# Kernel optimization log

Hardware: AMD Instinct MI355X
Metric: run time of the kernel (lower is better)

## Reference

```python
import jax, jax.numpy as jnp
import numpy as np

L, V, D, S_MAX, B, S, H = 8, 32000, 1024, 1024, 4, 1024, 16
FF = 4 * D
EPS = 1e-5


def setup_inputs() -> dict:
    key = jax.random.key(0)
    ks = jax.random.split(key, 20)
    g = lambda k, shape: jax.random.normal(k, shape, dtype=jnp.float32) * 0.02
    inp = {
        'tokens': jax.random.randint(ks[0], (B, S), 0, V, dtype=jnp.int32),
        'num_heads': H,
        'emb': g(ks[1], (V, D)),
        'pos_emb': g(ks[2], (S_MAX, D)),
        'Wq': g(ks[3], (L, D, D)), 'bq': jnp.zeros((L, D), jnp.float32),
        'Wk': g(ks[4], (L, D, D)), 'bk': jnp.zeros((L, D), jnp.float32),
        'Wv': g(ks[5], (L, D, D)), 'bv': jnp.zeros((L, D), jnp.float32),
        'Wo': g(ks[6], (L, D, D)), 'bo': jnp.zeros((L, D), jnp.float32),
        'n1_s': jnp.ones((L, D), jnp.float32), 'n1_b': jnp.zeros((L, D), jnp.float32),
        'W1': g(ks[7], (L, D, FF)), 'b1': jnp.zeros((L, FF), jnp.float32),
        'W2': g(ks[8], (L, FF, D)), 'b2': jnp.zeros((L, D), jnp.float32),
        'n2_s': jnp.ones((L, D), jnp.float32), 'n2_b': jnp.zeros((L, D), jnp.float32),
    }
    return inp


def _layernorm(x, s, b):
    mu = jnp.mean(x, axis=-1, keepdims=True)
    var = jnp.mean(jnp.square(x - mu), axis=-1, keepdims=True)
    return s * (x - mu) * jax.lax.rsqrt(var + EPS) + b


def _forward(tokens, num_heads, emb, pos_emb, Wq, bq, Wk, bk, Wv, bv, Wo, bo,
             n1_s, n1_b, W1, b1, W2, b2, n2_s, n2_b):
    Bn, Sn = tokens.shape
    d = emb.shape[1]
    hd = d // num_heads
    x = emb[tokens] + pos_emb[:Sn][None, :, :]  # [B,S,D]

    def split_heads(t):  # [B,S,D] -> [B,H,S,hd]
        return t.reshape(Bn, Sn, num_heads, hd).transpose(0, 2, 1, 3)

    causal = jnp.triu(jnp.ones((Sn, Sn), dtype=bool), k=1)
    scale = 1.0 / np.sqrt(hd)
    nlayers = Wq.shape[0]
    for l in range(nlayers):
        q = split_heads(x @ Wq[l] + bq[l])
        k = split_heads(x @ Wk[l] + bk[l])
        v = split_heads(x @ Wv[l] + bv[l])
        scores = jnp.einsum('bhqd,bhkd->bhqk', q, k) * scale
        scores = jnp.where(causal, -jnp.inf, scores)
        attn = jax.nn.softmax(scores, axis=-1)
        ctx = jnp.einsum('bhqk,bhkd->bhqd', attn, v)
        ctx = ctx.transpose(0, 2, 1, 3).reshape(Bn, Sn, d)
        x = _layernorm(x + (ctx @ Wo[l] + bo[l]), n1_s[l], n1_b[l])
        h = jax.nn.relu(x @ W1[l] + b1[l])
        x = _layernorm(x + (h @ W2[l] + b2[l]), n2_s[l], n2_b[l])
    return x @ emb.T  # tied output head -> [B,S,V]


def reference(tokens, num_heads, emb, pos_emb, Wq, bq, Wk, bk, Wv, bv, Wo, bo,
              n1_s, n1_b, W1, b1, W2, b2, n2_s, n2_b):
    return _forward(tokens, num_heads, emb, pos_emb, Wq, bq, Wk, bk, Wv, bv,
                    Wo, bo, n1_s, n1_b, W1, b1, W2, b2, n2_s, n2_b)
```

## Files before the change

### kernel.cpp

```cpp
#include <hip/hip_runtime.h>

#define D_MODEL 1024
#define SEQ     1024
#define BATCH   4
#define NHEAD   16
#define HDIM    64
#define FF_DIM  4096
#define NLAYER  8
#define VOCAB   32000
#define ROWS    (BATCH*SEQ)
#define QKV_N   3072
#define LN_EPS  1e-5f

typedef __attribute__((ext_vector_type(4))) float   f32x4;
typedef __attribute__((ext_vector_type(8))) unsigned short u16x8;
typedef __attribute__((ext_vector_type(8))) __bf16  bf16x8;

typedef const unsigned int __attribute__((address_space(1)))* gas_t;
typedef unsigned int __attribute__((address_space(3)))* las_t;

__device__ __forceinline__ void gld16(const void* g, void* l) {
    __builtin_amdgcn_global_load_lds((gas_t)g, (las_t)l, 16, 0, 0);
}

__device__ __forceinline__ unsigned short f2bf(float f) {
    unsigned int u = __builtin_bit_cast(unsigned int, f);
    u += 0x7FFFu + ((u >> 16) & 1u);
    return (unsigned short)(u >> 16);
}

__device__ __forceinline__ float bf2f(unsigned short u) {
    return __builtin_bit_cast(float, (unsigned int)u << 16);
}

__device__ __forceinline__ f32x4 mfma32(u16x8 a, u16x8 b, f32x4 c) {
    return __builtin_amdgcn_mfma_f32_16x16x32_bf16(
        __builtin_bit_cast(bf16x8, a), __builtin_bit_cast(bf16x8, b), c, 0, 0, 0);
}

__global__ __launch_bounds__(256) void embed_k(
    const int* __restrict__ tok, const float* __restrict__ emb,
    const float* __restrict__ pos, unsigned short* __restrict__ xb)
{
    int bs = blockIdx.x;
    int s  = bs & (SEQ - 1);
    int tk = tok[bs];
    int c  = threadIdx.x * 4;
    float4 e = *(const float4*)(emb + (size_t)tk * D_MODEL + c);
    float4 p = *(const float4*)(pos + (size_t)s * D_MODEL + c);
    float y0 = e.x + p.x, y1 = e.y + p.y, y2 = e.z + p.z, y3 = e.w + p.w;
    size_t base = (size_t)bs * D_MODEL + c;
    unsigned long long pk = (unsigned long long)f2bf(y0)
        | ((unsigned long long)f2bf(y1) << 16)
        | ((unsigned long long)f2bf(y2) << 32)
        | ((unsigned long long)f2bf(y3) << 48);
    *(unsigned long long*)(xb + base) = pk;
}

__global__ __launch_bounds__(256) void cast_bf(
    const float* __restrict__ in, unsigned short* __restrict__ out, size_t n)
{
    size_t i = ((size_t)blockIdx.x * 256 + threadIdx.x) * 4;
    if (i >= n) return;
    float4 v = *(const float4*)(in + i);
    unsigned long long pk = (unsigned long long)f2bf(v.x)
        | ((unsigned long long)f2bf(v.y) << 16)
        | ((unsigned long long)f2bf(v.z) << 32)
        | ((unsigned long long)f2bf(v.w) << 48);
    *(unsigned long long*)(out + i) = pk;
}

__global__ __launch_bounds__(256) void bias3_k(
    const float* __restrict__ bq, const float* __restrict__ bk,
    const float* __restrict__ bv, float* __restrict__ out)
{
    int l = blockIdx.x / 3, which = blockIdx.x % 3;
    const float* src = which == 0 ? bq : (which == 1 ? bk : bv);
    int i = threadIdx.x * 4;
    float4 v = *(const float4*)(src + (size_t)l * D_MODEL + i);
    *(float4*)(out + (size_t)l * QKV_N + which * D_MODEL + i) = v;
}

__device__ __forceinline__ void tc_tile(
    const float* __restrict__ W, unsigned short* __restrict__ Wt,
    int K, int N, int n0, int k0)
{
    __shared__ float t[64][65];
    int rr = threadIdx.x >> 4;
    int cc = (threadIdx.x & 15) * 4;
#pragma unroll
    for (int it = 0; it < 4; it++) {
        int r = it * 16 + rr;
        float4 v = *(const float4*)(W + (size_t)(k0 + r) * N + n0 + cc);
        t[r][cc] = v.x; t[r][cc + 1] = v.y; t[r][cc + 2] = v.z; t[r][cc + 3] = v.w;
    }
    __syncthreads();
#pragma unroll
    for (int it = 0; it < 4; it++) {
        int n = it * 16 + rr;
        unsigned long long pk = (unsigned long long)f2bf(t[cc][n])
            | ((unsigned long long)f2bf(t[cc + 1][n]) << 16)
            | ((unsigned long long)f2bf(t[cc + 2][n]) << 32)
            | ((unsigned long long)f2bf(t[cc + 3][n]) << 48);
        *(unsigned long long*)(Wt + (size_t)(n0 + n) * K + k0 + cc) = pk;
    }
}

__global__ __launch_bounds__(256) void transpose_all(
    const float* __restrict__ Wq, const float* __restrict__ Wk,
    const float* __restrict__ Wv, const float* __restrict__ Wo,
    const float* __restrict__ W1, const float* __restrict__ W2,
    unsigned short* __restrict__ wt)
{
    int b = blockIdx.x;
    const float* W; unsigned short* out; int K, N, t;
    if (b < 768)       { int w = b >> 8; t = b & 255; W = w == 0 ? Wq : (w == 1 ? Wk : Wv);
                         out = wt + (size_t)w * 1048576; K = 1024; N = 1024; }
    else if (b < 1024) { t = b - 768;  W = Wo; out = wt + (size_t)3 * 1048576; K = 1024; N = 1024; }
    else if (b < 2048) { t = b - 1024; W = W1; out = wt + (size_t)4 * 1048576; K = 1024; N = 4096; }
    else               { t = b - 2048; W = W2; out = wt + (size_t)8 * 1048576; K = 4096; N = 1024; }
    int ntx = N >> 6;
    tc_tile(W, out, K, N, (t % ntx) * 64, (t / ntx) * 64);
}

template<int MODE>
__global__ __launch_bounds__(256, 3) void gemm_bt(
    const unsigned short* __restrict__ A, int lda,
    const unsigned short* __restrict__ Bt, int ldb,
    const float* __restrict__ bias, void* __restrict__ Cout, int N, int Klen)
{
    __shared__ unsigned short As[128 * 32];
    __shared__ unsigned short Bs[128 * 32];
    const int part = blockIdx.y;
    A  += (size_t)part * Klen;
    Bt += (size_t)part * Klen;
    int flat = blockIdx.x;
    const int bm = flat & 31, bn = flat >> 5;
    const int tid  = threadIdx.x;
    const int wid  = tid >> 6, lane = tid & 63;
    const int l16  = lane & 15, lhi = lane >> 4;
    const int wr   = wid >> 1, wc = wid & 1;

    const int srow = wid * 32 + (lane >> 2);
    const int scol = (lane & 3) * 8;
    const unsigned short* gA0 = A  + ((size_t)bm * 128 + srow) * lda + scol;
    const unsigned short* gB0 = Bt + ((size_t)bn * 128 + srow) * ldb + scol;
    unsigned short* lA = As + wid * 32 * 32;
    unsigned short* lB = Bs + wid * 32 * 32;

    f32x4 acc[4][4];
#pragma unroll
    for (int i = 0; i < 4; i++)
#pragma unroll
        for (int j = 0; j < 4; j++) acc[i][j] = (f32x4){0.f, 0.f, 0.f, 0.f};

    for (int k0 = 0; k0 < Klen; k0 += 32) {
        __syncthreads();
        gld16(gA0 + k0,                    lA);
        gld16(gA0 + k0 + 16 * (size_t)lda, lA + 16 * 32);
        gld16(gB0 + k0,                    lB);
        gld16(gB0 + k0 + 16 * (size_t)ldb, lB + 16 * 32);
        __syncthreads();
        u16x8 af[4], bfr[4];
#pragma unroll
        for (int i = 0; i < 4; i++)
            af[i] = *(const u16x8*)(As + (wr * 64 + i * 16 + l16) * 32 + lhi * 8);
#pragma unroll
        for (int i = 0; i < 4; i++)
            bfr[i] = *(const u16x8*)(Bs + (wc * 64 + i * 16 + l16) * 32 + lhi * 8);
#pragma unroll
        for (int mi = 0; mi < 4; mi++)
#pragma unroll
            for (int ni = 0; ni < 4; ni++)
                acc[mi][ni] = mfma32(af[mi], bfr[ni], acc[mi][ni]);
    }

    const size_t pofs = (size_t)part * (size_t)ROWS * N;
#pragma unroll
    for (int mi = 0; mi < 4; mi++) {
        float bv[4];
#pragma unroll
        for (int ni = 0; ni < 4; ni++)
            bv[ni] = (bias && part == 0) ? bias[bn * 128 + wc * 64 + ni * 16 + l16] : 0.f;
#pragma unroll
        for (int j = 0; j < 4; j++) {
            int row = bm * 128 + wr * 64 + mi * 16 + lhi * 4 + j;
#pragma unroll
            for (int ni = 0; ni < 4; ni++) {
                int col = bn * 128 + wc * 64 + ni * 16 + l16;
                float v = acc[mi][ni][j] + bv[ni];
                size_t idx = pofs + (size_t)row * N + col;
                if constexpr (MODE == 1) {
                    ((unsigned short*)Cout)[idx] = f2bf(v);
                } else {
                    ((unsigned short*)Cout)[idx] = f2bf(v > 0.f ? v : 0.f);
                }
            }
        }
    }
}

#define PSYNC() do { __builtin_amdgcn_s_barrier(); \
    asm volatile("s_waitcnt lgkmcnt(0)" ::: "memory"); \
    __builtin_amdgcn_sched_barrier(0); } while (0)
#define PEND() __builtin_amdgcn_s_barrier()
#define VM4()  asm volatile("s_waitcnt vmcnt(4)" ::: "memory")

#define LOADA(reg, half) do { \
    _Pragma("unroll") \
    for (int m_ = 0; m_ < 4; m_++) { \
        aF[m_][0] = *(const u16x8*)((reg) + ((half)*4 + m_) * 2048 + lane0); \
        aF[m_][1] = *(const u16x8*)((reg) + ((half)*4 + m_) * 2048 + lane1); \
    } } while (0)

#define LOADB(reg, np) do { \
    _Pragma("unroll") \
    for (int n_ = 0; n_ < 2; n_++) { \
        bF[(np)*2 + n_][0] = *(const u16x8*)((reg) + ((np)*2 + n_) * 2048 + lane0); \
        bF[(np)*2 + n_][1] = *(const u16x8*)((reg) + ((np)*2 + n_) * 2048 + lane1); \
    } } while (0)

#define MFMA8(ma, np) do { \
    __builtin_amdgcn_s_setprio(1); \
    _Pragma("unroll") \
    for (int m_ = 0; m_ < 4; m_++) \
        _Pragma("unroll") \
        for (int n_ = 0; n_ < 2; n_++) { \
            acc[(ma)+m_][(np)*2+n_] = mfma32(aF[m_][0], bF[(np)*2+n_][0], acc[(ma)+m_][(np)*2+n_]); \
            acc[(ma)+m_][(np)*2+n_] = mfma32(aF[m_][1], bF[(np)*2+n_][1], acc[(ma)+m_][(np)*2+n_]); \
        } \
    __builtin_amdgcn_s_setprio(0); \
} while (0)

template<int MODE, int SWZ>
__global__ __launch_bounds__(512, 2) void gemm256(
    const unsigned short* __restrict__ A, int lda,
    const unsigned short* __restrict__ Bt, int ldb,
    const float* __restrict__ bias, void* __restrict__ Cout, int N, int Klen)
{
    __shared__ unsigned short lds[65536] __attribute__((aligned(128)));
    const int tid = threadIdx.x, wid = tid >> 6, lane = tid & 63;
    const int l16 = lane & 15, lhi = lane >> 4;
    const int wr = wid >> 2, wc = wid & 3;

    const int part = blockIdx.y;
    A  += (size_t)part * Klen;
    Bt += (size_t)part * Klen;

    int flat = blockIdx.x;
    if constexpr (SWZ) {
        int cpx = gridDim.x >> 3; flat = (flat & 7) * cpx + (flat >> 3);
    }
    const int bm = flat & 15, bn = flat >> 4;
    const int NT = Klen >> 6;

    const int srowL = tid >> 3;
    const int scolb = ((tid & 7) << 4) ^ (((tid >> 3) & 7) << 4);
    const unsigned short* baseA = A  + (size_t)(bm * 256 + srowL) * lda + (scolb >> 1);
    const unsigned short* baseB = Bt + (size_t)(bn * 256 + srowL) * ldb + (scolb >> 1);
    unsigned short* dst0 = lds + wid * 512;

    auto stage = [&](int isB, int tile, int h) {
        const size_t ld = isB ? (size_t)ldb : (size_t)lda;
        const unsigned short* s = (isB ? baseB : baseA) + (size_t)(h * 128) * ld + (size_t)tile * 64;
        unsigned short* d = dst0 + (tile & 1) * 32768 + isB * 16384 + h * 8192;
        gld16(s, d);
        gld16(s + 64 * ld, d + 4096);
    };

    const int lswz  = (l16 & 7) << 4;
    const int lane0 = ((lhi * 16) ^ lswz) + l16 * 128;
    const int lane1 = ((64 + lhi * 16) ^ lswz) + l16 * 128;

    const char* aR0 = (const char*)lds + wr * 16384;
    const char* bR0 = (const char*)lds + 32768 + (wc >> 1) * 16384 + (wc & 1) * 8192;
    const char* aR1 = aR0 + 65536;
    const char* bR1 = bR0 + 65536;

    f32x4 acc[8][4];
#pragma unroll
    for (int i = 0; i < 8; i++)
#pragma unroll
        for (int j = 0; j < 4; j++) acc[i][j] = (f32x4){0.f, 0.f, 0.f, 0.f};
    u16x8 aF[4][2], bF[4][2];

    stage(1, 0, 0); stage(1, 0, 1);
    stage(0, 0, 0); stage(0, 0, 1);
    stage(1, 1, 0); stage(1, 1, 1);
    VM4();
    __builtin_amdgcn_s_barrier();

    for (int t = 0; t < NT; t += 2) {
        const bool more = (t + 2) < NT;
        LOADA(aR0, 0); LOADB(bR0, 0); stage(0, t + 1, 0);
        PSYNC(); MFMA8(0, 0); PEND();
        LOADB(bR0, 1);                stage(0, t + 1, 1);
        PSYNC(); MFMA8(0, 1); PEND();
        LOADA(aR0, 1);                if (more) stage(1, t + 2, 0);
        PSYNC(); MFMA8(4, 0); PEND();
        if (more) { stage(1, t + 2, 1); VM4(); }
        else      { asm volatile("s_waitcnt vmcnt(0)" ::: "memory"); }
        PSYNC(); MFMA8(4, 1); PEND();
        LOADA(aR1, 0); LOADB(bR1, 0); if (more) stage(0, t + 2, 0);
        PSYNC(); MFMA8(0, 0); PEND();
        LOADB(bR1, 1);                if (more) stage(0, t + 2, 1);
        PSYNC(); MFMA8(0, 1); PEND();
        LOADA(aR1, 1);                if (more) stage(1, t + 3, 0);
        PSYNC(); MFMA8(4, 0); PEND();
        if (more) { stage(1, t + 3, 1); VM4(); }
        PSYNC(); MFMA8(4, 1); PEND();
    }

    const size_t pofs = (size_t)part * (size_t)ROWS * N;
#pragma unroll
    for (int mi = 0; mi < 8; mi++) {
        float bv[4];
#pragma unroll
        for (int ni = 0; ni < 4; ni++)
            bv[ni] = (bias && part == 0) ? bias[bn * 256 + wc * 64 + ni * 16 + l16] : 0.f;
#pragma unroll
        for (int j = 0; j < 4; j++) {
            int row = bm * 256 + wr * 128 + mi * 16 + lhi * 4 + j;
#pragma unroll
            for (int ni = 0; ni < 4; ni++) {
                int col = bn * 256 + wc * 64 + ni * 16 + l16;
                float v = acc[mi][ni][j] + bv[ni];
                size_t idx = pofs + (size_t)row * N + col;
                if constexpr (MODE == 0) {
                    __builtin_nontemporal_store(v, (float*)Cout + idx);
                } else if constexpr (MODE == 1) {
                    ((unsigned short*)Cout)[idx] = f2bf(v);
                } else {
                    ((unsigned short*)Cout)[idx] = f2bf(v > 0.f ? v : 0.f);
                }
            }
        }
    }
}

__global__ __launch_bounds__(256, 3) void attn_fwd(
    const unsigned short* __restrict__ qkv, unsigned short* __restrict__ ctxb)
{
    __shared__ unsigned short Ks[64 * 72];
    __shared__ unsigned short Vs[64 * 72];
    __shared__ unsigned short Ps[4 * 16 * 72];
    const int tid = threadIdx.x;
    const int wid = tid >> 6, lane = tid & 63;
    const int l16 = lane & 15, lhi = lane >> 4;
    const int bh  = blockIdx.y, b = bh >> 4, h = bh & 15;
    const int p   = blockIdx.x;
    const int qA0 = p * 64;
    const int qB0 = (15 - p) * 64;
    const size_t rowbase = (size_t)b * SEQ;

    const unsigned short* qpA = qkv + (rowbase + qA0 + wid * 16 + l16) * QKV_N + h * HDIM + lhi * 8;
    u16x8 qAf0 = *(const u16x8*)qpA;
    u16x8 qAf1 = *(const u16x8*)(qpA + 32);
    const unsigned short* qpB = qkv + (rowbase + qB0 + wid * 16 + l16) * QKV_N + h * HDIM + lhi * 8;
    u16x8 qBf0 = *(const u16x8*)qpB;
    u16x8 qBf1 = *(const u16x8*)(qpB + 32);

    f32x4 oaA[4], oaB[4];
    float mjA[4], ljA[4], mjB[4], ljB[4];
#pragma unroll
    for (int i = 0; i < 4; i++) {
        oaA[i] = (f32x4){0.f, 0.f, 0.f, 0.f};
        oaB[i] = (f32x4){0.f, 0.f, 0.f, 0.f};
        mjA[i] = -1e30f; ljA[i] = 0.f;
        mjB[i] = -1e30f; ljB[i] = 0.f;
    }

    auto update = [&](u16x8 qf0, u16x8 qf1, f32x4 (&oa)[4],
                      float (&mj)[4], float (&lj)[4], int q0, int kv0) {
        f32x4 sa[4];
        __builtin_amdgcn_s_setprio(1);
#pragma unroll
        for (int ni = 0; ni < 4; ni++) {
            f32x4 z = (f32x4){0.f, 0.f, 0.f, 0.f};
            u16x8 k0f = *(const u16x8*)(&Ks[(ni * 16 + l16) * 72 + lhi * 8]);
            u16x8 k1f = *(const u16x8*)(&Ks[(ni * 16 + l16) * 72 + 32 + lhi * 8]);
            z = mfma32(qf0, k0f, z);
            z = mfma32(qf1, k1f, z);
            sa[ni] = z;
        }
        __builtin_amdgcn_s_setprio(0);
        float tm[4] = {-1e30f, -1e30f, -1e30f, -1e30f};
#pragma unroll
        for (int ni = 0; ni < 4; ni++)
#pragma unroll
            for (int j = 0; j < 4; j++) {
                float v = sa[ni][j] * 0.125f;
                int row = q0 + wid * 16 + lhi * 4 + j;
                int col = kv0 + ni * 16 + l16;
                if (col > row) v = -1e30f;
                sa[ni][j] = v;
                tm[j] = fmaxf(tm[j], v);
            }
#pragma unroll
        for (int j = 0; j < 4; j++) {
#pragma unroll
            for (int off = 1; off < 16; off <<= 1)
                tm[j] = fmaxf(tm[j], __shfl_xor(tm[j], off));
        }
        float al[4], rs[4] = {0.f, 0.f, 0.f, 0.f};
#pragma unroll
        for (int j = 0; j < 4; j++) {
            float mn = fmaxf(mj[j], tm[j]);
            al[j] = __expf(mj[j] - mn);
            mj[j] = mn;
        }
#pragma unroll
        for (int ni = 0; ni < 4; ni++)
#pragma unroll
            for (int j = 0; j < 4; j++) {
                float pv = __expf(sa[ni][j] - mj[j]);
                rs[j] += pv;
                Ps[wid * 1152 + (lhi * 4 + j) * 72 + ni * 16 + l16] = f2bf(pv);
            }
#pragma unroll
        for (int j = 0; j < 4; j++) {
#pragma unroll
            for (int off = 1; off < 16; off <<= 1)
                rs[j] += __shfl_xor(rs[j], off);
            lj[j] = lj[j] * al[j] + rs[j];
        }
#pragma unroll
        for (int di = 0; di < 4; di++)
#pragma unroll
            for (int j = 0; j < 4; j++) oa[di][j] *= al[j];
        __builtin_amdgcn_s_setprio(1);
#pragma unroll
        for (int di = 0; di < 4; di++) {
#pragma unroll
            for (int kc = 0; kc < 2; kc++) {
                u16x8 pf = *(const u16x8*)(&Ps[wid * 1152 + l16 * 72 + kc * 32 + lhi * 8]);
                u16x8 vf = *(const u16x8*)(&Vs[(di * 16 + l16) * 72 + kc * 32 + lhi * 8]);
                oa[di] = mfma32(pf, vf, oa[di]);
            }
        }
        __builtin_amdgcn_s_setprio(0);
    };

    const int ntB = 16 - p;
    for (int kt = 0; kt < ntB; ++kt) {
        const int kv0 = kt * 64;
        __syncthreads();
#pragma unroll
        for (int it = 0; it < 2; ++it) {
            int e = it * 256 + tid;
            int r = e >> 3, d0 = (e & 7) * 8;
            size_t goff = (rowbase + kv0 + r) * QKV_N + D_MODEL + h * HDIM + d0;
            u16x8 kk = *(const u16x8*)(qkv + goff);
            *(u16x8*)(&Ks[r * 72 + d0]) = kk;
        }
        if (tid < 128) {
            int r0 = (tid & 15) * 4, d0v = (tid >> 4) * 8;
            const unsigned short* vp = qkv + (rowbase + kv0 + r0) * QKV_N
                                       + 2 * D_MODEL + h * HDIM + d0v;
            u16x8 w0 = *(const u16x8*)vp;
            u16x8 w1 = *(const u16x8*)(vp + QKV_N);
            u16x8 w2 = *(const u16x8*)(vp + 2 * QKV_N);
            u16x8 w3 = *(const u16x8*)(vp + 3 * QKV_N);
#pragma unroll
            for (int j = 0; j < 8; j++) {
                unsigned long long pk = (unsigned long long)w0[j]
                    | ((unsigned long long)w1[j] << 16)
                    | ((unsigned long long)w2[j] << 32)
                    | ((unsigned long long)w3[j] << 48);
                *(unsigned long long*)(&Vs[(d0v + j) * 72 + r0]) = pk;
            }
        }
        __syncthreads();

        if (kt <= p) update(qAf0, qAf1, oaA, mjA, ljA, qA0, kv0);
        update(qBf0, qBf1, oaB, mjB, ljB, qB0, kv0);
    }

#pragma unroll
    for (int di = 0; di < 4; di++)
#pragma unroll
        for (int j = 0; j < 4; j++) {
            int rowA = qA0 + wid * 16 + lhi * 4 + j;
            ctxb[(rowbase + rowA) * D_MODEL + h * HDIM + di * 16 + l16] =
                f2bf(oaA[di][j] / ljA[j]);
            int rowB = qB0 + wid * 16 + lhi * 4 + j;
            ctxb[(rowbase + rowB) * D_MODEL + h * HDIM + di * 16 + l16] =
                f2bf(oaB[di][j] / ljB[j]);
        }
}

__global__ __launch_bounds__(256) void ln3(
    unsigned short* __restrict__ xb, const unsigned short* __restrict__ p0,
    const unsigned short* __restrict__ p1,
    const float* __restrict__ sc, const float* __restrict__ bi)
{
    const int row = blockIdx.x;
    const int t = threadIdx.x;
    const size_t base = (size_t)row * D_MODEL + t * 4;
    ushort4 xu = *(const ushort4*)(xb + base);
    ushort4 au = *(const ushort4*)(p0 + base);
    ushort4 bu = *(const ushort4*)(p1 + base);
    float v0 = bf2f(xu.x) + bf2f(au.x) + bf2f(bu.x);
    float v1 = bf2f(xu.y) + bf2f(au.y) + bf2f(bu.y);
    float v2 = bf2f(xu.z) + bf2f(au.z) + bf2f(bu.z);
    float v3 = bf2f(xu.w) + bf2f(au.w) + bf2f(bu.w);
    float sum = v0 + v1 + v2 + v3;
    float sq  = v0 * v0 + v1 * v1 + v2 * v2 + v3 * v3;
#pragma unroll
    for (int off = 1; off < 64; off <<= 1) {
        sum += __shfl_xor(sum, off);
        sq  += __shfl_xor(sq, off);
    }
    __shared__ float red[8];
    int wid = t >> 6, lane = t & 63;
    if (lane == 0) { red[wid] = sum; red[4 + wid] = sq; }
    __syncthreads();
    sum = red[0] + red[1] + red[2] + red[3];
    sq  = red[4] + red[5] + red[6] + red[7];
    float mu   = sum * (1.f / D_MODEL);
    float var  = sq * (1.f / D_MODEL) - mu * mu;
    float rstd = rsqrtf(var + LN_EPS);
    int c = t * 4;
    float4 sv = *(const float4*)(sc + c);
    float4 bv = *(const float4*)(bi + c);
    float y0 = sv.x * (v0 - mu) * rstd + bv.x;
    float y1 = sv.y * (v1 - mu) * rstd + bv.y;
    float y2 = sv.z * (v2 - mu) * rstd + bv.z;
    float y3 = sv.w * (v3 - mu) * rstd + bv.w;
    unsigned long long pk = (unsigned long long)f2bf(y0)
        | ((unsigned long long)f2bf(y1) << 16)
        | ((unsigned long long)f2bf(y2) << 32)
        | ((unsigned long long)f2bf(y3) << 48);
    *(unsigned long long*)(xb + base) = pk;
}

__global__ __launch_bounds__(256) void ln5(
    unsigned short* __restrict__ xb, const unsigned short* __restrict__ p,
    const float* __restrict__ sc, const float* __restrict__ bi)
{
    const int row = blockIdx.x;
    const int t = threadIdx.x;
    const size_t base = (size_t)row * D_MODEL + t * 4;
    const size_t stride = (size_t)ROWS * D_MODEL;
    ushort4 xu = *(const ushort4*)(xb + base);
    float v0 = bf2f(xu.x), v1 = bf2f(xu.y), v2 = bf2f(xu.z), v3 = bf2f(xu.w);
#pragma unroll
    for (int k = 0; k < 4; k++) {
        ushort4 pu = *(const ushort4*)(p + k * stride + base);
        v0 += bf2f(pu.x); v1 += bf2f(pu.y); v2 += bf2f(pu.z); v3 += bf2f(pu.w);
    }
    float sum = v0 + v1 + v2 + v3;
    float sq  = v0 * v0 + v1 * v1 + v2 * v2 + v3 * v3;
#pragma unroll
    for (int off = 1; off < 64; off <<= 1) {
        sum += __shfl_xor(sum, off);
        sq  += __shfl_xor(sq, off);
    }
    __shared__ float red[8];
    int wid = t >> 6, lane = t & 63;
    if (lane == 0) { red[wid] = sum; red[4 + wid] = sq; }
    __syncthreads();
    sum = red[0] + red[1] + red[2] + red[3];
    sq  = red[4] + red[5] + red[6] + red[7];
    float mu   = sum * (1.f / D_MODEL);
    float var  = sq * (1.f / D_MODEL) - mu * mu;
    float rstd = rsqrtf(var + LN_EPS);
    int c = t * 4;
    float4 sv = *(const float4*)(sc + c);
    float4 bv = *(const float4*)(bi + c);
    float y0 = sv.x * (v0 - mu) * rstd + bv.x;
    float y1 = sv.y * (v1 - mu) * rstd + bv.y;
    float y2 = sv.z * (v2 - mu) * rstd + bv.z;
    float y3 = sv.w * (v3 - mu) * rstd + bv.w;
    unsigned long long pk = (unsigned long long)f2bf(y0)
        | ((unsigned long long)f2bf(y1) << 16)
        | ((unsigned long long)f2bf(y2) << 32)
        | ((unsigned long long)f2bf(y3) << 48);
    *(unsigned long long*)(xb + base) = pk;
}

extern "C" void kernel_launch(void* const* d_in, const int* in_sizes, int n_in,
                              void* d_out, int out_size, void* d_ws, size_t ws_size,
                              hipStream_t stream)
{
    (void)in_sizes; (void)n_in; (void)out_size;
    const int*   tokens = (const int*)d_in[0];
    const float* emb  = (const float*)d_in[2];
    const float* pose = (const float*)d_in[3];
    const float* Wq = (const float*)d_in[4];
    const float* bq = (const float*)d_in[5];
    const float* Wk = (const float*)d_in[6];
    const float* bk = (const float*)d_in[7];
    const float* Wv = (const float*)d_in[8];
    const float* bv = (const float*)d_in[9];
    const float* Wo = (const float*)d_in[10];
    const float* bo = (const float*)d_in[11];
    const float* n1s = (const float*)d_in[12];
    const float* n1b = (const float*)d_in[13];
    const float* W1 = (const float*)d_in[14];
    const float* b1 = (const float*)d_in[15];
    const float* W2 = (const float*)d_in[16];
    const float* b2 = (const float*)d_in[17];
    const float* n2s = (const float*)d_in[18];
    const float* n2b = (const float*)d_in[19];

    char* w = (char*)d_ws;
    size_t off = 0;
    auto carve = [&](size_t bytes) -> void* {
        void* p = w + off;
        off = (off + bytes + 255) & ~(size_t)255;
        return p;
    };
    unsigned short* tmp = (unsigned short*)carve((size_t)4 * ROWS * D_MODEL * 2);
    unsigned short* xb    = (unsigned short*)carve((size_t)ROWS * D_MODEL * 2);
    unsigned short* qkvb  = (unsigned short*)carve((size_t)ROWS * QKV_N * 2);
    unsigned short* cbuf  = (unsigned short*)carve((size_t)ROWS * D_MODEL * 2);
    unsigned short* hbuf  = (unsigned short*)carve((size_t)ROWS * FF_DIM * 2);
    unsigned short* wt = (unsigned short*)carve((size_t)12 * 1048576 * 2);
    float* bqkv = (float*)carve((size_t)NLAYER * QKV_N * 4);
    unsigned short* embb = qkvb;
    unsigned short* tmp1 = tmp + (size_t)ROWS * D_MODEL;
    if (off > ws_size) return;

    bias3_k<<<NLAYER * 3, 256, 0, stream>>>(bq, bk, bv, bqkv);
    embed_k<<<ROWS, 256, 0, stream>>>(tokens, emb, pose, xb);

    for (int l = 0; l < NLAYER; l++) {
        unsigned short* wtQKV = wt;
        unsigned short* wtWo  = wt + (size_t)3 * 1048576;
        unsigned short* wtW1  = wt + (size_t)4 * 1048576;
        unsigned short* wtW2  = wt + (size_t)8 * 1048576;

        transpose_all<<<3072, 256, 0, stream>>>(
            Wq + (size_t)l * D_MODEL * D_MODEL, Wk + (size_t)l * D_MODEL * D_MODEL,
            Wv + (size_t)l * D_MODEL * D_MODEL, Wo + (size_t)l * D_MODEL * D_MODEL,
            W1 + (size_t)l * D_MODEL * FF_DIM,  W2 + (size_t)l * FF_DIM * D_MODEL, wt);

        gemm256<1, 1><<<dim3((QKV_N / 256) * 16, 1), 512, 0, stream>>>(
            xb, D_MODEL, wtQKV, D_MODEL, bqkv + (size_t)l * QKV_N, qkvb, QKV_N, D_MODEL);

        attn_fwd<<<dim3(8, BATCH * NHEAD), 256, 0, stream>>>(qkvb, cbuf);

        gemm_bt<1><<<dim3(256, 2), 256, 0, stream>>>(cbuf, D_MODEL, wtWo, D_MODEL,
                                                     bo + (size_t)l * D_MODEL, tmp, D_MODEL, D_MODEL / 2);
        ln3<<<ROWS, 256, 0, stream>>>(xb, tmp, tmp1, n1s + (size_t)l * D_MODEL, n1b + (size_t)l * D_MODEL);

        gemm256<2, 1><<<dim3((FF_DIM / 256) * 16, 1), 512, 0, stream>>>(
            xb, D_MODEL, wtW1, D_MODEL, b1 + (size_t)l * FF_DIM, hbuf, FF_DIM, D_MODEL);
        gemm256<1, 1><<<dim3((D_MODEL / 256) * 16, 4), 512, 0, stream>>>(
            hbuf, FF_DIM, wtW2, FF_DIM, b2 + (size_t)l * D_MODEL, tmp, D_MODEL, FF_DIM / 4);
        ln5<<<ROWS, 256, 0, stream>>>(xb, tmp, n2s + (size_t)l * D_MODEL, n2b + (size_t)l * D_MODEL);
    }

    cast_bf<<<(VOCAB * D_MODEL) / 1024, 256, 0, stream>>>(emb, embb, (size_t)VOCAB * D_MODEL);
    gemm256<0, 0><<<dim3((VOCAB / 256) * 16, 1), 512, 0, stream>>>(
        xb, D_MODEL, embb, D_MODEL, nullptr, d_out, VOCAB, D_MODEL);
}
```

Measured before the change: 1.958 ms.

## Double-buffer K/V tiles in attention with register prefetch of next tile

```diff
diff --git a/kernel.cpp b/kernel.cpp
--- a/kernel.cpp
+++ b/kernel.cpp
@@ -341,8 +341,8 @@
 __global__ __launch_bounds__(256, 3) void attn_fwd(
     const unsigned short* __restrict__ qkv, unsigned short* __restrict__ ctxb)
 {
-    __shared__ unsigned short Ks[64 * 72];
-    __shared__ unsigned short Vs[64 * 72];
+    __shared__ unsigned short Ks[2][64 * 72];
+    __shared__ unsigned short Vs[2][64 * 72];
     __shared__ unsigned short Ps[4 * 16 * 72];
     const int tid = threadIdx.x;
     const int wid = tid >> 6, lane = tid & 63;
@@ -370,15 +370,47 @@
         mjB[i] = -1e30f; ljB[i] = 0.f;
     }
 
+    const int kr0r = tid >> 3,         kr0d = (tid & 7) * 8;
+    const int kr1r = (256 + tid) >> 3, kr1d = (tid & 7) * 8;
+    const int vr0  = (tid & 15) * 4,   vd0  = (tid >> 4) * 8;
+    u16x8 kp0, kp1, vp0, vp1, vp2, vp3;
+
+    auto ldKV = [&](int kv0) {
+        kp0 = *(const u16x8*)(qkv + (rowbase + kv0 + kr0r) * QKV_N + D_MODEL + h * HDIM + kr0d);
+        kp1 = *(const u16x8*)(qkv + (rowbase + kv0 + kr1r) * QKV_N + D_MODEL + h * HDIM + kr1d);
+        if (tid < 128) {
+            const unsigned short* vp = qkv + (rowbase + kv0 + vr0) * QKV_N
+                                       + 2 * D_MODEL + h * HDIM + vd0;
+            vp0 = *(const u16x8*)vp;
+            vp1 = *(const u16x8*)(vp + QKV_N);
+            vp2 = *(const u16x8*)(vp + 2 * QKV_N);
+            vp3 = *(const u16x8*)(vp + 3 * QKV_N);
+        }
+    };
+    auto wrKV = [&](int buf) {
+        *(u16x8*)(&Ks[buf][kr0r * 72 + kr0d]) = kp0;
+        *(u16x8*)(&Ks[buf][kr1r * 72 + kr1d]) = kp1;
+        if (tid < 128) {
+#pragma unroll
+            for (int j = 0; j < 8; j++) {
+                unsigned long long pk = (unsigned long long)vp0[j]
+                    | ((unsigned long long)vp1[j] << 16)
+                    | ((unsigned long long)vp2[j] << 32)
+                    | ((unsigned long long)vp3[j] << 48);
+                *(unsigned long long*)(&Vs[buf][(vd0 + j) * 72 + vr0]) = pk;
+            }
+        }
+    };
+
     auto update = [&](u16x8 qf0, u16x8 qf1, f32x4 (&oa)[4],
-                      float (&mj)[4], float (&lj)[4], int q0, int kv0) {
+                      float (&mj)[4], float (&lj)[4], int q0, int kv0, int buf) {
         f32x4 sa[4];
         __builtin_amdgcn_s_setprio(1);
 #pragma unroll
         for (int ni = 0; ni < 4; ni++) {
             f32x4 z = (f32x4){0.f, 0.f, 0.f, 0.f};
-            u16x8 k0f = *(const u16x8*)(&Ks[(ni * 16 + l16) * 72 + lhi * 8]);
-            u16x8 k1f = *(const u16x8*)(&Ks[(ni * 16 + l16) * 72 + 32 + lhi * 8]);
+            u16x8 k0f = *(const u16x8*)(&Ks[buf][(ni * 16 + l16) * 72 + lhi * 8]);
+            u16x8 k1f = *(const u16x8*)(&Ks[buf][(ni * 16 + l16) * 72 + 32 + lhi * 8]);
             z = mfma32(qf0, k0f, z);
             z = mfma32(qf1, k1f, z);
             sa[ni] = z;
@@ -434,7 +466,7 @@
 #pragma unroll
             for (int kc = 0; kc < 2; kc++) {
                 u16x8 pf = *(const u16x8*)(&Ps[wid * 1152 + l16 * 72 + kc * 32 + lhi * 8]);
-                u16x8 vf = *(const u16x8*)(&Vs[(di * 16 + l16) * 72 + kc * 32 + lhi * 8]);
+                u16x8 vf = *(const u16x8*)(&Vs[buf][(di * 16 + l16) * 72 + kc * 32 + lhi * 8]);
                 oa[di] = mfma32(pf, vf, oa[di]);
             }
         }
@@ -442,38 +474,17 @@
     };
 
     const int ntB = 16 - p;
+    ldKV(0);
+    wrKV(0);
+    __syncthreads();
     for (int kt = 0; kt < ntB; ++kt) {
+        const int buf = kt & 1;
         const int kv0 = kt * 64;
+        if (kt + 1 < ntB) ldKV(kv0 + 64);
+        if (kt <= p) update(qAf0, qAf1, oaA, mjA, ljA, qA0, kv0, buf);
+        update(qBf0, qBf1, oaB, mjB, ljB, qB0, kv0, buf);
+        if (kt + 1 < ntB) wrKV(buf ^ 1);
         __syncthreads();
-#pragma unroll
-        for (int it = 0; it < 2; ++it) {
-            int e = it * 256 + tid;
-            int r = e >> 3, d0 = (e & 7) * 8;
-            size_t goff = (rowbase + kv0 + r) * QKV_N + D_MODEL + h * HDIM + d0;
-            u16x8 kk = *(const u16x8*)(qkv + goff);
-            *(u16x8*)(&Ks[r * 72 + d0]) = kk;
-        }
-        if (tid < 128) {
-            int r0 = (tid & 15) * 4, d0v = (tid >> 4) * 8;
-            const unsigned short* vp = qkv + (rowbase + kv0 + r0) * QKV_N
-                                       + 2 * D_MODEL + h * HDIM + d0v;
-            u16x8 w0 = *(const u16x8*)vp;
-            u16x8 w1 = *(const u16x8*)(vp + QKV_N);
-            u16x8 w2 = *(const u16x8*)(vp + 2 * QKV_N);
-            u16x8 w3 = *(const u16x8*)(vp + 3 * QKV_N);
-#pragma unroll
-            for (int j = 0; j < 8; j++) {
-                unsigned long long pk = (unsigned long long)w0[j]
-                    | ((unsigned long long)w1[j] << 16)
-                    | ((unsigned long long)w2[j] << 32)
-                    | ((unsigned long long)w3[j] << 48);
-                *(unsigned long long*)(&Vs[(d0v + j) * 72 + r0]) = pk;
-            }
-        }
-        __syncthreads();
-
-        if (kt <= p) update(qAf0, qAf1, oaA, mjA, ljA, qA0, kv0);
-        update(qBf0, qBf1, oaB, mjB, ljB, qB0, kv0);
     }
 
 #pragma unroll
```

Result: faster. 1.888 ms (-3.6%).
